# Kernel optimization log

Hardware: AMD Instinct MI355X
Metric: run time of the kernel (lower is better)

The kernel has to match this reference:

```python
import jax, jax.numpy as jnp
import numpy as np
import math

B, T, F = 1024, 120, 32          # batch, lookback, num_features
D, H, L = 128, 4, 2              # model_dim, heads, encoder layers
SD, RD, M, HOR = 16, 8, 5, 90    # symbol_dim, regime_dim, num_target_metrics, horizon
NSYM = 5000
HD = D // H

def _p(k, shape, scale=0.02):
    return (jax.random.normal(k, shape) * scale).astype(jnp.float32)

def _sinusoidal(seq_len, d_model):
    pos = jnp.arange(seq_len, dtype=jnp.float32)[:, None]
    div = jnp.exp(jnp.arange(0, d_model, 2, dtype=jnp.float32) * (-math.log(10000.0) / d_model))
    pe = jnp.zeros((seq_len, d_model), jnp.float32)
    pe = pe.at[:, 0::2].set(jnp.sin(pos * div))
    pe = pe.at[:, 1::2].set(jnp.cos(pos * div))
    return pe

def _ln(x, w, b, eps=1e-5):
    m = x.mean(-1, keepdims=True)
    v = jnp.var(x, axis=-1, keepdims=True)
    return (x - m) * jax.lax.rsqrt(v + eps) * w + b

def _mha(x, wqkv, bqkv, wo, bo):
    b, t, d = x.shape
    qkv = x @ wqkv.T + bqkv                      # [B,T,3D]
    q, k, v = jnp.split(qkv, 3, axis=-1)
    heads = lambda u: u.reshape(b, t, H, HD).transpose(0, 2, 1, 3)
    q, k, v = heads(q), heads(k), heads(v)       # [B,H,T,HD]
    s = jnp.einsum('bhqd,bhkd->bhqk', q, k) / jnp.sqrt(jnp.float32(HD))
    a = jax.nn.softmax(s, axis=-1)
    o = jnp.einsum('bhqk,bhkd->bhqd', a, v).transpose(0, 2, 1, 3).reshape(b, t, d)
    return o @ wo.T + bo

def setup_inputs():
    ks = iter(jax.random.split(jax.random.key(0), 40))
    return {
        'x': jax.random.normal(next(ks), (B, T, F), jnp.float32),
        'sym_id': jax.random.randint(next(ks), (B,), 0, NSYM),
        'regime_id': jax.random.randint(next(ks), (B,), 0, 3),
        'sym_emb': _p(next(ks), (NSYM, SD), 1.0),
        'reg_emb': _p(next(ks), (3, RD), 1.0),
        'in_w': _p(next(ks), (D, F + SD)), 'in_b': jnp.zeros((D,), jnp.float32),
        'enc_qkv_w': _p(next(ks), (L, 3 * D, D)), 'enc_qkv_b': jnp.zeros((L, 3 * D), jnp.float32),
        'enc_out_w': _p(next(ks), (L, D, D)), 'enc_out_b': jnp.zeros((L, D), jnp.float32),
        'enc_ln1_w': jnp.ones((L, D), jnp.float32), 'enc_ln1_b': jnp.zeros((L, D), jnp.float32),
        'enc_ln2_w': jnp.ones((L, D), jnp.float32), 'enc_ln2_b': jnp.zeros((L, D), jnp.float32),
        'enc_f1_w': _p(next(ks), (L, 4 * D, D)), 'enc_f1_b': jnp.zeros((L, 4 * D), jnp.float32),
        'enc_f2_w': _p(next(ks), (L, D, 4 * D)), 'enc_f2_b': jnp.zeros((L, D), jnp.float32),
        'pool_w': _p(next(ks), (1, D)), 'pool_b': jnp.zeros((1,), jnp.float32),
        'ctx_w': _p(next(ks), (D, D + SD + RD)), 'ctx_b': jnp.zeros((D,), jnp.float32),
        'gru_wih': _p(next(ks), (3 * D, M + D)), 'gru_whh': _p(next(ks), (3 * D, D)),
        'gru_bih': jnp.zeros((3 * D,), jnp.float32), 'gru_bhh': jnp.zeros((3 * D,), jnp.float32),
        'mu_w1': _p(next(ks), (64, D)), 'mu_b1': jnp.zeros((64,), jnp.float32),
        'mu_w2': _p(next(ks), (M, 64)), 'mu_b2': jnp.zeros((M,), jnp.float32),
        'vol_w1': _p(next(ks), (64, D)), 'vol_b1': jnp.zeros((64,), jnp.float32),
        'vol_w2': _p(next(ks), (M, 64)), 'vol_b2': jnp.zeros((M,), jnp.float32),
    }

def reference(x, sym_id, regime_id, sym_emb, reg_emb, in_w, in_b,
              enc_qkv_w, enc_qkv_b, enc_out_w, enc_out_b,
              enc_ln1_w, enc_ln1_b, enc_ln2_w, enc_ln2_b,
              enc_f1_w, enc_f1_b, enc_f2_w, enc_f2_b,
              pool_w, pool_b, ctx_w, ctx_b,
              gru_wih, gru_whh, gru_bih, gru_bhh,
              mu_w1, mu_b1, mu_w2, mu_b2, vol_w1, vol_b1, vol_w2, vol_b2):
    b = x.shape[0]
    se = sym_emb[sym_id]                                        # [B,SD]
    sym_seq = jnp.broadcast_to(se[:, None, :], (b, T, SD))
    feats = jnp.concatenate([x, sym_seq], axis=-1) @ in_w.T + in_b
    feats = feats + _sinusoidal(T, D)[None]
    # pre-LN transformer encoder (PyTorch norm_first=True, relu FFN, eval mode: no dropout)
    h = feats
    for l in range(L):
        y = _ln(h, enc_ln1_w[l], enc_ln1_b[l])
        h = h + _mha(y, enc_qkv_w[l], enc_qkv_b[l], enc_out_w[l], enc_out_b[l])
        y = _ln(h, enc_ln2_w[l], enc_ln2_b[l])
        h = h + (jax.nn.relu(y @ enc_f1_w[l].T + enc_f1_b[l]) @ enc_f2_w[l].T + enc_f2_b[l])
    attn_w = jax.nn.softmax(h @ pool_w.T + pool_b, axis=1)      # softmax over time
    pooled = (attn_w * h).sum(axis=1)                           # [B,D]
    re = reg_emb[regime_id]
    ctx = jnp.concatenate([pooled, se, re], axis=-1) @ ctx_w.T + ctx_b
    rv = jnp.std(x[:, :, 0], axis=1, ddof=1, keepdims=True)     # unbiased std like torch.std, [B,1]
    gelu = lambda t: jax.nn.gelu(t, approximate=False)          # torch nn.GELU default (erf)

    def step_fn(carry, _):
        hd, step = carry
        gi = jnp.concatenate([step, ctx], axis=-1) @ gru_wih.T + gru_bih
        gh = hd @ gru_whh.T + gru_bhh
        ir, iz, inn = jnp.split(gi, 3, axis=-1)
        hr, hz, hn = jnp.split(gh, 3, axis=-1)
        r = jax.nn.sigmoid(ir + hr)
        z = jax.nn.sigmoid(iz + hz)
        n = jnp.tanh(inn + r * hn)
        hd = (1.0 - z) * n + z * hd
        mu = jnp.tanh(gelu(hd @ mu_w1.T + mu_b1) @ mu_w2.T + mu_b2)
        sig = jax.nn.softplus(gelu(hd @ vol_w1.T + vol_b1) @ vol_w2.T + vol_b2) * (1.0 + rv)
        pred = mu * sig
        return (hd, pred), pred

    (_, _), preds = jax.lax.scan(step_fn, (ctx, jnp.zeros((b, M), x.dtype)), None, length=HOR)
    return preds.transpose(1, 0, 2)                             # [B,HOR,M]
```

## Files before the change

### kernel.cpp

```cpp
#include <hip/hip_runtime.h>
#include <math.h>

typedef __bf16 bf16;
typedef __bf16 bf16x8 __attribute__((ext_vector_type(8)));
typedef __bf16 bf16x2 __attribute__((ext_vector_type(2)));
typedef float  floatx4 __attribute__((ext_vector_type(4)));

#define BB 1024
#define TT 120
#define FF 32
#define DD 128
#define NROWS (BB*TT)
#define HOR 90
#define MM 5

__device__ __forceinline__ float fast_sigmoid(float x) {
    x = fminf(fmaxf(x, -30.f), 30.f);
    return 1.f / (1.f + __expf(-x));
}
__device__ __forceinline__ float fast_tanh(float x) {
    x = fminf(fmaxf(x, -15.f), 15.f);
    float e = __expf(-2.f * x);
    return (1.f - e) / (1.f + e);
}

__global__ __launch_bounds__(256) void prep_weights(
    const float* __restrict__ qkv, const float* __restrict__ outw,
    const float* __restrict__ f1,  const float* __restrict__ f2,
    bf16* __restrict__ dst)
{
    int i = blockIdx.x*256 + threadIdx.x;
    if (i >= 393216) return;
    float v;
    if      (i < 98304)  v = qkv[i];
    else if (i < 131072) v = outw[i - 98304];
    else if (i < 262144) v = f1[i - 131072];
    else                 v = f2[i - 262144];
    dst[i] = (bf16)v;
}

__global__ __launch_bounds__(256) void inproj3(
    const float* __restrict__ x, const int* __restrict__ sym_id,
    const float* __restrict__ sym_emb, const float* __restrict__ in_w,
    const float* __restrict__ in_b, const float* __restrict__ lnw,
    const float* __restrict__ lnb, float* __restrict__ h, bf16* __restrict__ y)
{
    __shared__ float xin[4][48];
    const int tid = threadIdx.x, lane = tid & 63, wave = tid >> 6;
    const int row0 = blockIdx.x * 4;
    if (tid < 192) {
        int rr = tid / 48, k = tid % 48;
        int row = row0 + rr;
        int b = row / TT;
        xin[rr][k] = (k < 32) ? x[(size_t)row*FF + k]
                              : sym_emb[(size_t)sym_id[b]*16 + (k - 32)];
    }
    __syncthreads();
    const int row = row0 + wave;
    const int t = row % TT;
    const int d0 = lane*2;
    float a0 = in_b[d0], a1 = in_b[d0+1];
    const float* w0 = in_w + (size_t)d0*48;
    const float* w1 = w0 + 48;
    #pragma unroll 8
    for (int k = 0; k < 48; ++k) {
        float xv = xin[wave][k];
        a0 += xv * w0[k];
        a1 += xv * w1[k];
    }
    const float f = expf((float)d0 * (-9.210340371976184f / 128.f));
    const float arg = (float)t * f;
    a0 += sinf(arg);
    a1 += cosf(arg);
    float2 hv = {a0, a1};
    *(float2*)&h[(size_t)row*DD + d0] = hv;
    float s = a0 + a1, ss = a0*a0 + a1*a1;
    #pragma unroll
    for (int o = 1; o < 64; o <<= 1) { s += __shfl_xor(s, o); ss += __shfl_xor(ss, o); }
    float mean = s * (1.f/128.f);
    float var  = ss * (1.f/128.f) - mean*mean;
    float rstd = rsqrtf(var + 1e-5f);
    bf16x2 o2 = {(bf16)((a0 - mean)*rstd*lnw[d0]   + lnb[d0]),
                 (bf16)((a1 - mean)*rstd*lnw[d0+1] + lnb[d0+1])};
    *(bf16x2*)&y[(size_t)row*DD + d0] = o2;
}

template<int EPI>
__global__ __launch_bounds__(256) void gemm64(
    const bf16* __restrict__ A, const bf16* __restrict__ W,
    const float* __restrict__ bias, const float* __restrict__ res,
    void* __restrict__ outp, const float* __restrict__ lnw,
    const float* __restrict__ lnb, bf16* __restrict__ yout, int N, int K)
{
    __shared__ alignas(16) bf16 As[128*64];
    __shared__ alignas(16) bf16 Ws[128*64];
    __shared__ float psum[2][128];
    __shared__ float psq[2][128];
    const int tid = threadIdx.x;
    const int lane = tid & 63, wave = tid >> 6;
    const int q = lane >> 4, ml = lane & 15;
    const int wm = (wave & 1) * 64, wn = (wave >> 1) * 64;
    const int m0 = blockIdx.x * 128, n0 = blockIdx.y * 128;
    floatx4 acc[4][4];
    #pragma unroll
    for (int i = 0; i < 4; ++i)
        #pragma unroll
        for (int j = 0; j < 4; ++j) acc[i][j] = (floatx4){0.f,0.f,0.f,0.f};
    const int nkb = K >> 6;
    for (int kb = 0; kb < nkb; ++kb) {
        #pragma unroll
        for (int i = 0; i < 4; ++i) {
            int idx = i*256 + tid;
            int r = idx >> 3, c = idx & 7;
            int sw = ((c ^ (r & 7)) * 8);
            *(uint4*)&As[r*64 + sw] = *(const uint4*)(A + (size_t)(m0 + r)*K + kb*64 + c*8);
            *(uint4*)&Ws[r*64 + sw] = *(const uint4*)(W + (size_t)(n0 + r)*K + kb*64 + c*8);
        }
        __syncthreads();
        #pragma unroll
        for (int s = 0; s < 2; ++s) {
            bf16x8 af[4], bfr[4];
            #pragma unroll
            for (int t = 0; t < 4; ++t) {
                int ra = wm + t*16 + ml;
                af[t]  = *(const bf16x8*)&As[ra*64 + (((s*4+q) ^ (ra & 7))*8)];
                int rb = wn + t*16 + ml;
                bfr[t] = *(const bf16x8*)&Ws[rb*64 + (((s*4+q) ^ (rb & 7))*8)];
            }
            #pragma unroll
            for (int i = 0; i < 4; ++i)
                #pragma unroll
                for (int j = 0; j < 4; ++j)
                    acc[i][j] = __builtin_amdgcn_mfma_f32_16x16x32_bf16(af[i], bfr[j], acc[i][j], 0, 0, 0);
        }
        __syncthreads();
    }
    #pragma unroll
    for (int j = 0; j < 4; ++j) {
        int col = n0 + wn + j*16 + ml;
        float bv = bias[col];
        #pragma unroll
        for (int i = 0; i < 4; ++i) {
            #pragma unroll
            for (int r = 0; r < 4; ++r) {
                int row = m0 + wm + i*16 + q*4 + r;
                size_t o = (size_t)row * N + col;
                float v = acc[i][j][r] + bv;
                if      (EPI == 0) ((bf16*)outp)[o] = (bf16)v;
                else if (EPI == 1) ((bf16*)outp)[o] = (bf16)fmaxf(v, 0.f);
                else {
                    v += res[o];
                    ((float*)outp)[o] = v;
                    acc[i][j][r] = v;
                }
            }
        }
    }
    if (EPI == 3) {
        float lw[4], lb[4];
        #pragma unroll
        for (int j = 0; j < 4; ++j) { int col = wn + j*16 + ml; lw[j] = lnw[col]; lb[j] = lnb[col]; }
        #pragma unroll
        for (int i = 0; i < 4; ++i)
            #pragma unroll
            for (int r = 0; r < 4; ++r) {
                float s  = acc[i][0][r] + acc[i][1][r] + acc[i][2][r] + acc[i][3][r];
                float ss = acc[i][0][r]*acc[i][0][r] + acc[i][1][r]*acc[i][1][r]
                         + acc[i][2][r]*acc[i][2][r] + acc[i][3][r]*acc[i][3][r];
                #pragma unroll
                for (int o = 1; o < 16; o <<= 1) { s += __shfl_xor(s, o); ss += __shfl_xor(ss, o); }
                if (ml == 0) {
                    int row = wm + i*16 + q*4 + r;
                    psum[wn >> 6][row] = s;
                    psq [wn >> 6][row] = ss;
                }
            }
        __syncthreads();
        #pragma unroll
        for (int i = 0; i < 4; ++i)
            #pragma unroll
            for (int r = 0; r < 4; ++r) {
                int row = wm + i*16 + q*4 + r;
                float mean = (psum[0][row] + psum[1][row]) * (1.f/128.f);
                float var  = (psq[0][row] + psq[1][row]) * (1.f/128.f) - mean*mean;
                float rstd = rsqrtf(var + 1e-5f);
                #pragma unroll
                for (int j = 0; j < 4; ++j) {
                    int col = wn + j*16 + ml;
                    yout[(size_t)(m0 + row)*128 + col] =
                        (bf16)((acc[i][j][r] - mean)*rstd*lw[j] + lb[j]);
                }
            }
    }
}

template<int LNFUSE>
__global__ __launch_bounds__(256) void ffn_fused(
    const bf16* __restrict__ y, const bf16* __restrict__ W1,
    const float* __restrict__ b1, const bf16* __restrict__ W2,
    const float* __restrict__ b2, float* __restrict__ h,
    const float* __restrict__ lnw, const float* __restrict__ lnb,
    bf16* __restrict__ yout)
{
    __shared__ alignas(16) bf16 ys[64*128];
    __shared__ alignas(16) bf16 mid[4][64*128];
    __shared__ alignas(16) bf16 wbuf[128*128];
    const int tid = threadIdx.x;
    const int lane = tid & 63, wave = tid >> 6;
    const int q = lane >> 4, ml = lane & 15;
    const int wm = wave * 16;
    const int m0 = blockIdx.x * 64;
    #pragma unroll
    for (int i = 0; i < 4; ++i) {
        int idx = i*256 + tid;
        int r = idx >> 4, cc = idx & 15;
        *(uint4*)&ys[r*128 + ((cc ^ (r & 15))*8)] =
            *(const uint4*)(y + (size_t)(m0 + r)*128 + cc*8);
    }
    __syncthreads();
    for (int nb = 0; nb < 4; ++nb) {
        #pragma unroll
        for (int i = 0; i < 8; ++i) {
            int idx = i*256 + tid;
            int r = idx >> 4, cc = idx & 15;
            *(uint4*)&wbuf[r*128 + ((cc ^ (r & 15))*8)] =
                *(const uint4*)(W1 + (size_t)(nb*128 + r)*128 + cc*8);
        }
        __syncthreads();
        bf16x8 af[4];
        #pragma unroll
        for (int s = 0; s < 4; ++s) {
            int ra = wm + ml;
            af[s] = *(const bf16x8*)&ys[ra*128 + (((4*s+q) ^ (ra & 15))*8)];
        }
        #pragma unroll
        for (int j = 0; j < 8; ++j) {
            floatx4 acc = (floatx4){0.f,0.f,0.f,0.f};
            #pragma unroll
            for (int s = 0; s < 4; ++s) {
                int rb = j*16 + ml;
                bf16x8 bfr = *(const bf16x8*)&wbuf[rb*128 + (((4*s+q) ^ (rb & 15))*8)];
                acc = __builtin_amdgcn_mfma_f32_16x16x32_bf16(af[s], bfr, acc, 0, 0, 0);
            }
            int col = j*16 + ml;
            float bv = b1[nb*128 + col];
            #pragma unroll
            for (int r = 0; r < 4; ++r) {
                int row = wm + q*4 + r;
                float v = fmaxf(acc[r] + bv, 0.f);
                mid[nb][row*128 + (((col>>3) ^ (row & 15))*8) + (col & 7)] = (bf16)v;
            }
        }
        __syncthreads();
    }
    floatx4 acc2[8];
    #pragma unroll
    for (int j = 0; j < 8; ++j) acc2[j] = (floatx4){0.f,0.f,0.f,0.f};
    for (int kb = 0; kb < 4; ++kb) {
        #pragma unroll
        for (int i = 0; i < 8; ++i) {
            int idx = i*256 + tid;
            int r = idx >> 4, cc = idx & 15;
            *(uint4*)&wbuf[r*128 + ((cc ^ (r & 15))*8)] =
                *(const uint4*)(W2 + (size_t)r*512 + kb*128 + cc*8);
        }
        __syncthreads();
        bf16x8 af[4];
        #pragma unroll
        for (int s = 0; s < 4; ++s) {
            int ra = wm + ml;
            af[s] = *(const bf16x8*)&mid[kb][ra*128 + (((4*s+q) ^ (ra & 15))*8)];
        }
        #pragma unroll
        for (int j = 0; j < 8; ++j) {
            #pragma unroll
            for (int s = 0; s < 4; ++s) {
                int rb = j*16 + ml;
                bf16x8 bfr = *(const bf16x8*)&wbuf[rb*128 + (((4*s+q) ^ (rb & 15))*8)];
                acc2[j] = __builtin_amdgcn_mfma_f32_16x16x32_bf16(af[s], bfr, acc2[j], 0, 0, 0);
            }
        }
        __syncthreads();
    }
    float vr[8][4];
    #pragma unroll
    for (int j = 0; j < 8; ++j) {
        int col = j*16 + ml;
        float bv = b2[col];
        #pragma unroll
        for (int r = 0; r < 4; ++r) {
            int row = wm + q*4 + r;
            size_t o = (size_t)(m0 + row)*128 + col;
            float v = acc2[j][r] + bv + h[o];
            h[o] = v;
            vr[j][r] = v;
        }
    }
    if (LNFUSE) {
        float lw[8], lb[8];
        #pragma unroll
        for (int j = 0; j < 8; ++j) { lw[j] = lnw[j*16 + ml]; lb[j] = lnb[j*16 + ml]; }
        #pragma unroll
        for (int r = 0; r < 4; ++r) {
            float s = 0.f, ss = 0.f;
            #pragma unroll
            for (int j = 0; j < 8; ++j) { s += vr[j][r]; ss += vr[j][r]*vr[j][r]; }
            #pragma unroll
            for (int o = 1; o < 16; o <<= 1) { s += __shfl_xor(s, o); ss += __shfl_xor(ss, o); }
            float mean = s * (1.f/128.f);
            float var  = ss * (1.f/128.f) - mean*mean;
            float rstd = rsqrtf(var + 1e-5f);
            int row = wm + q*4 + r;
            #pragma unroll
            for (int j = 0; j < 8; ++j)
                yout[(size_t)(m0 + row)*128 + j*16 + ml] =
                    (bf16)((vr[j][r] - mean)*rstd*lw[j] + lb[j]);
        }
    }
}

__global__ __launch_bounds__(256) void attn_b16(
    const bf16* __restrict__ qkv, bf16* __restrict__ O)
{
    __shared__ alignas(16) bf16 Qs[128*32];
    __shared__ alignas(16) bf16 Ks[128*32];
    __shared__ alignas(16) bf16 VT[32*128];
    __shared__ float Sf[64*132];
    const int tid = threadIdx.x, lane = tid & 63, wave = tid >> 6;
    const int q = lane >> 4, ml = lane & 15;
    const int b = blockIdx.x >> 2, hh = blockIdx.x & 3;
    const bf16* base = qkv + (size_t)b*TT*384 + hh*32;
    #pragma unroll
    for (int i = 0; i < 2; ++i) {
        int idx = i*256 + tid;
        int r = idx >> 2, cc = idx & 3;
        uint4 vq = {0,0,0,0}, vk = {0,0,0,0};
        if (r < TT) {
            vq = *(const uint4*)(base + (size_t)r*384 + cc*8);
            vk = *(const uint4*)(base + (size_t)r*384 + 128 + cc*8);
        }
        int cs = cc ^ ((r >> 1) & 3);
        *(uint4*)&Qs[r*32 + cs*8] = vq;
        *(uint4*)&Ks[r*32 + cs*8] = vk;
    }
    #pragma unroll
    for (int i = 0; i < 16; ++i) {
        int idx = i*256 + tid;
        int t = idx >> 5, e = idx & 31;
        bf16 v = (bf16)0.f;
        if (t < TT) v = base[(size_t)t*384 + 256 + e];
        VT[e*128 + (((t >> 3) ^ (e & 15))*8) + (t & 7)] = v;
    }
    __syncthreads();
    const float scale = 0.17677669529663687f;
    for (int hf = 0; hf < 2; ++hf) {
        {
            int rowa = hf*64 + wave*16 + ml;
            bf16x8 af = *(const bf16x8*)&Qs[rowa*32 + ((q ^ ((rowa>>1)&3))*8)];
            #pragma unroll
            for (int ni = 0; ni < 8; ++ni) {
                int rowb = ni*16 + ml;
                bf16x8 bfr = *(const bf16x8*)&Ks[rowb*32 + ((q ^ ((rowb>>1)&3))*8)];
                floatx4 a4 = __builtin_amdgcn_mfma_f32_16x16x32_bf16(
                    af, bfr, (floatx4){0.f,0.f,0.f,0.f}, 0, 0, 0);
                #pragma unroll
                for (int r = 0; r < 4; ++r)
                    Sf[(wave*16 + q*4 + r)*132 + ni*16 + ml] = a4[r]*scale;
            }
        }
        __syncthreads();
        {
            int rl = wave*16 + (lane >> 2);
            int part = lane & 3;
            int rg = hf*64 + rl;
            if (rg < TT) {
                float* rowp = &Sf[rl*132 + part*30];
                float mx = -3e38f;
                #pragma unroll 10
                for (int j = 0; j < 30; ++j) mx = fmaxf(mx, rowp[j]);
                mx = fmaxf(mx, __shfl_xor(mx, 1));
                mx = fmaxf(mx, __shfl_xor(mx, 2));
                float sm = 0.f;
                #pragma unroll 10
                for (int j = 0; j < 30; ++j) sm += __expf(rowp[j] - mx);
                sm += __shfl_xor(sm, 1);
                sm += __shfl_xor(sm, 2);
                float inv = 1.f / sm;
                #pragma unroll 10
                for (int j = 0; j < 30; ++j) rowp[j] = __expf(rowp[j] - mx) * inv;
                if (part == 3) {
                    #pragma unroll
                    for (int c = 120; c < 128; ++c) Sf[rl*132 + c] = 0.f;
                }
            }
        }
        __syncthreads();
        floatx4 pacc[2];
        pacc[0] = (floatx4){0.f,0.f,0.f,0.f};
        pacc[1] = (floatx4){0.f,0.f,0.f,0.f};
        #pragma unroll
        for (int s = 0; s < 4; ++s) {
            const float* pr = &Sf[(wave*16 + ml)*132 + 32*s + 8*q];
            float4 p0 = *(const float4*)pr;
            float4 p1 = *(const float4*)(pr + 4);
            bf16x8 af2 = {(bf16)p0.x,(bf16)p0.y,(bf16)p0.z,(bf16)p0.w,
                          (bf16)p1.x,(bf16)p1.y,(bf16)p1.z,(bf16)p1.w};
            #pragma unroll
            for (int nv = 0; nv < 2; ++nv) {
                int e = nv*16 + ml;
                bf16x8 bfr = *(const bf16x8*)&VT[e*128 + ((((4*s+q) ^ (e & 15)))*8)];
                pacc[nv] = __builtin_amdgcn_mfma_f32_16x16x32_bf16(af2, bfr, pacc[nv], 0, 0, 0);
            }
        }
        #pragma unroll
        for (int nv = 0; nv < 2; ++nv)
            #pragma unroll
            for (int r = 0; r < 4; ++r) {
                int row = hf*64 + wave*16 + q*4 + r;
                if (row < TT)
                    O[((size_t)b*TT + row)*DD + hh*32 + nv*16 + ml] = (bf16)pacc[nv][r];
            }
        __syncthreads();
    }
}

__global__ __launch_bounds__(128) void pool_ctx3(
    const float* __restrict__ h, const float* __restrict__ x,
    const int* __restrict__ sym_id, const int* __restrict__ regime_id,
    const float* __restrict__ sym_emb, const float* __restrict__ reg_emb,
    const float* __restrict__ pool_w, const float* __restrict__ pool_b,
    const float* __restrict__ ctx_w, const float* __restrict__ ctx_b,
    float* __restrict__ ctxf, float* __restrict__ rv)
{
    __shared__ float sc[120];
    __shared__ float aw[120];
    __shared__ float cat[152];
    const int b = blockIdx.x;
    const int tid = threadIdx.x, lane = tid & 63, wave = tid >> 6;
    const float* hb = h + (size_t)b*TT*DD;
    for (int t = wave*60; t < wave*60 + 60; ++t) {
        const float2* hp = (const float2*)(hb + t*DD);
        float2 v = hp[lane];
        float s = v.x * pool_w[lane*2] + v.y * pool_w[lane*2 + 1];
        #pragma unroll
        for (int o = 1; o < 64; o <<= 1) s += __shfl_xor(s, o);
        if (lane == 0) sc[t] = s + pool_b[0];
    }
    __syncthreads();
    if (wave == 0) {
        float v0 = sc[lane];
        float v1 = (lane < 56) ? sc[lane + 64] : -3e38f;
        float mx = fmaxf(v0, v1);
        #pragma unroll
        for (int o = 1; o < 64; o <<= 1) mx = fmaxf(mx, __shfl_xor(mx, o));
        float e0 = expf(v0 - mx);
        float e1 = (lane < 56) ? expf(v1 - mx) : 0.f;
        float sm = e0 + e1;
        #pragma unroll
        for (int o = 1; o < 64; o <<= 1) sm += __shfl_xor(sm, o);
        float inv = 1.f / sm;
        aw[lane] = e0 * inv;
        if (lane < 56) aw[lane + 64] = e1 * inv;
    } else {
        float v0 = x[((size_t)b*TT + lane)*FF];
        float v1 = (lane < 56) ? x[((size_t)b*TT + lane + 64)*FF] : 0.f;
        float s = v0 + v1;
        #pragma unroll
        for (int o = 1; o < 64; o <<= 1) s += __shfl_xor(s, o);
        float mean = s / 120.f;
        float d0 = v0 - mean, d1 = (lane < 56) ? (v1 - mean) : 0.f;
        float ss = d0*d0 + d1*d1;
        #pragma unroll
        for (int o = 1; o < 64; o <<= 1) ss += __shfl_xor(ss, o);
        if (lane == 0) rv[b] = sqrtf(ss / 119.f);
    }
    __syncthreads();
    {
        float p = 0.f;
        for (int t = 0; t < TT; ++t) p += aw[t] * hb[(size_t)t*DD + tid];
        cat[tid] = p;
    }
    if (tid < 16)      cat[128 + tid] = sym_emb[(size_t)sym_id[b]*16 + tid];
    else if (tid < 24) cat[144 + (tid-16)] = reg_emb[regime_id[b]*8 + (tid-16)];
    __syncthreads();
    float acc = ctx_b[tid];
    const float* wr = ctx_w + (size_t)tid*152;
    for (int j = 0; j < 152; ++j) acc += cat[j] * wr[j];
    ctxf[(size_t)b*128 + tid] = acc;
}

#define G1IDX(rr,c) ((rr)*132 + (c) + ((c)>>5))
__global__ __launch_bounds__(512, 1) void gru5_kernel(
    const float* __restrict__ ctxf, const float* __restrict__ wih,
    const float* __restrict__ bih, const float* __restrict__ whh,
    const float* __restrict__ bhh,
    const float* __restrict__ mu_w1, const float* __restrict__ mu_b1,
    const float* __restrict__ mu_w2, const float* __restrict__ mu_b2,
    const float* __restrict__ vol_w1, const float* __restrict__ vol_b1,
    const float* __restrict__ vol_w2, const float* __restrict__ vol_b2,
    const float* __restrict__ rv, float* __restrict__ out)
{
    __shared__ alignas(16) bf16 hdh[2][16*128];
    __shared__ alignas(16) bf16 hdl[2][16*128];
    __shared__ float g1_s[16*132];
    __shared__ float step_s[80];
    __shared__ float w2m_s[320], w2v_s[320];
    __shared__ float rvv[16];
    const int tid = threadIdx.x, lane = tid & 63, wave = tid >> 6;
    const int q = lane >> 4, ml = lane & 15;
    const int col = wave*16 + ml;
    const int r0 = blockIdx.x * 16;

    bf16x8 wbh1[3][4], wbl1[3][4], wbh2[4], wbl2[4];
    float w50[5], w51[5], w52[5];
    #pragma unroll
    for (int g = 0; g < 3; ++g) {
        int n = g*128 + col;
        #pragma unroll
        for (int s = 0; s < 4; ++s) {
            const float* wp = whh + (size_t)n*128 + s*32 + q*8;
            float4 f0 = *(const float4*)wp;
            float4 f1 = *(const float4*)(wp + 4);
            float v[8] = {f0.x,f0.y,f0.z,f0.w,f1.x,f1.y,f1.z,f1.w};
            bf16x8 hi, lo;
            #pragma unroll
            for (int j = 0; j < 8; ++j) {
                bf16 hb = (bf16)v[j]; hi[j] = hb; lo[j] = (bf16)(v[j] - (float)hb);
            }
            wbh1[g][s] = hi; wbl1[g][s] = lo;
        }
        #pragma unroll
        for (int j = 0; j < 5; ++j) {
            float wv = wih[(size_t)n*133 + j];
            if (g == 0) w50[j] = wv; else if (g == 1) w51[j] = wv; else w52[j] = wv;
        }
    }
    const float bhh0 = bhh[col], bhh1 = bhh[128 + col], bhh2 = bhh[256 + col];
    float bias2 = (col < 64) ? mu_b1[col] : vol_b1[col - 64];
    #pragma unroll
    for (int s = 0; s < 4; ++s) {
        const float* wp = ((col < 64) ? (mu_w1 + (size_t)col*128)
                                      : (vol_w1 + (size_t)(col-64)*128)) + s*32 + q*8;
        float4 f0 = *(const float4*)wp;
        float4 f1 = *(const float4*)(wp + 4);
        float v[8] = {f0.x,f0.y,f0.z,f0.w,f1.x,f1.y,f1.z,f1.w};
        bf16x8 hi, lo;
        #pragma unroll
        for (int j = 0; j < 8; ++j) {
            bf16 hb = (bf16)v[j]; hi[j] = hb; lo[j] = (bf16)(v[j] - (float)hb);
        }
        wbh2[s] = hi; wbl2[s] = lo;
    }

    for (int i = tid; i < 2048; i += 512) {
        int rr = i >> 7, d = i & 127;
        float v = ctxf[(size_t)r0*128 + i];
        g1_s[G1IDX(rr, d)] = v;
        int pos = rr*128 + (((d>>3) ^ rr) & 15)*8 + (d & 7);
        bf16 hb = (bf16)v;
        hdh[0][pos] = hb;
        hdl[0][pos] = (bf16)(v - (float)hb);
    }
    for (int i = tid; i < 320; i += 512) { w2m_s[i] = mu_w2[i]; w2v_s[i] = vol_w2[i]; }
    if (tid < 80) step_s[tid] = 0.f;
    if (tid < 16) rvv[tid] = 1.f + rv[r0 + tid];
    __syncthreads();
    float gi0[4], gi1[4], gi2[4];
    #pragma unroll
    for (int g = 0; g < 3; ++g) {
        int n = g*128 + col;
        const float* wr = wih + (size_t)n*133 + 5;
        #pragma unroll
        for (int r = 0; r < 4; ++r) {
            int row = q*4 + r;
            float a = bih[n];
            #pragma unroll 4
            for (int k = 0; k < 128; ++k) a += g1_s[G1IDX(row, k)] * wr[k];
            if (g == 0) gi0[r] = a; else if (g == 1) gi1[r] = a; else gi2[r] = a;
        }
    }
    __syncthreads();

    int cur = 0;
    for (int st = 0; st < HOR; ++st) {
        const int nxt = cur ^ 1;
        {
            bf16x8 ah[4], al[4];
            #pragma unroll
            for (int s = 0; s < 4; ++s) {
                int off = ml*128 + (((s*4 + q) ^ ml) & 15)*8;
                ah[s] = *(const bf16x8*)&hdh[cur][off];
                al[s] = *(const bf16x8*)&hdl[cur][off];
            }
            floatx4 a1 = (floatx4){0,0,0,0}, a2 = (floatx4){0,0,0,0}, a3 = (floatx4){0,0,0,0};
            floatx4 b1 = (floatx4){0,0,0,0}, b2 = (floatx4){0,0,0,0}, b3 = (floatx4){0,0,0,0};
            floatx4 c1 = (floatx4){0,0,0,0}, c2 = (floatx4){0,0,0,0}, c3 = (floatx4){0,0,0,0};
            #pragma unroll
            for (int s = 0; s < 4; ++s) {
                a1 = __builtin_amdgcn_mfma_f32_16x16x32_bf16(ah[s], wbh1[0][s], a1, 0, 0, 0);
                a2 = __builtin_amdgcn_mfma_f32_16x16x32_bf16(ah[s], wbl1[0][s], a2, 0, 0, 0);
                a3 = __builtin_amdgcn_mfma_f32_16x16x32_bf16(al[s], wbh1[0][s], a3, 0, 0, 0);
                b1 = __builtin_amdgcn_mfma_f32_16x16x32_bf16(ah[s], wbh1[1][s], b1, 0, 0, 0);
                b2 = __builtin_amdgcn_mfma_f32_16x16x32_bf16(ah[s], wbl1[1][s], b2, 0, 0, 0);
                b3 = __builtin_amdgcn_mfma_f32_16x16x32_bf16(al[s], wbh1[1][s], b3, 0, 0, 0);
                c1 = __builtin_amdgcn_mfma_f32_16x16x32_bf16(ah[s], wbh1[2][s], c1, 0, 0, 0);
                c2 = __builtin_amdgcn_mfma_f32_16x16x32_bf16(ah[s], wbl1[2][s], c2, 0, 0, 0);
                c3 = __builtin_amdgcn_mfma_f32_16x16x32_bf16(al[s], wbh1[2][s], c3, 0, 0, 0);
            }
            floatx4 ar = a1 + a2 + a3;
            floatx4 az = b1 + b2 + b3;
            floatx4 an = c1 + c2 + c3;
            #pragma unroll
            for (int r = 0; r < 4; ++r) {
                int row = q*4 + r;
                float ir = gi0[r], iz = gi1[r], in_ = gi2[r];
                #pragma unroll
                for (int j = 0; j < 5; ++j) {
                    float sv = step_s[row*5 + j];
                    ir  += sv * w50[j];
                    iz  += sv * w51[j];
                    in_ += sv * w52[j];
                }
                float rg = fast_sigmoid(ir + ar[r] + bhh0);
                float zg = fast_sigmoid(iz + az[r] + bhh1);
                float nn = fast_tanh(in_ + rg*(an[r] + bhh2));
                int pos = row*128 + (((col>>3) ^ row) & 15)*8 + (col & 7);
                float hold = (float)hdh[cur][pos] + (float)hdl[cur][pos];
                float hnew = (1.f - zg)*nn + zg*hold;
                bf16 hb = (bf16)hnew;
                hdh[nxt][pos] = hb;
                hdl[nxt][pos] = (bf16)(hnew - (float)hb);
            }
        }
        __syncthreads();
        {
            bf16x8 ah[4], al[4];
            #pragma unroll
            for (int s = 0; s < 4; ++s) {
                int off = ml*128 + (((s*4 + q) ^ ml) & 15)*8;
                ah[s] = *(const bf16x8*)&hdh[nxt][off];
                al[s] = *(const bf16x8*)&hdl[nxt][off];
            }
            floatx4 d1 = (floatx4){0,0,0,0}, d2 = (floatx4){0,0,0,0}, d3 = (floatx4){0,0,0,0};
            #pragma unroll
            for (int s = 0; s < 4; ++s) {
                d1 = __builtin_amdgcn_mfma_f32_16x16x32_bf16(ah[s], wbh2[s], d1, 0, 0, 0);
                d2 = __builtin_amdgcn_mfma_f32_16x16x32_bf16(ah[s], wbl2[s], d2, 0, 0, 0);
                d3 = __builtin_amdgcn_mfma_f32_16x16x32_bf16(al[s], wbh2[s], d3, 0, 0, 0);
            }
            floatx4 a4 = d1 + d2 + d3;
            #pragma unroll
            for (int r = 0; r < 4; ++r) {
                float u = a4[r] + bias2;
                g1_s[G1IDX(q*4 + r, col)] = 0.5f*u*(1.f + erff(u*0.70710678118654752f));
            }
        }
        __syncthreads();
        if (tid < 320) {
            int g = tid >> 2;
            int sub = tid & 3;
            int head = sub >> 1, half = sub & 1;
            int rr = g / 5, o = g % 5;
            const float* w2 = head ? w2v_s : w2m_s;
            int wb = o*64 + half*32;
            int gb = head*64 + half*32;
            float s = 0.f;
            #pragma unroll 8
            for (int j = 0; j < 32; ++j)
                s += g1_s[G1IDX(rr, gb + j)] * w2[wb + j];
            s += __shfl_xor(s, 1);
            float resv;
            if (head == 0) resv = tanhf(s + mu_b2[o]);
            else {
                float av = s + vol_b2[o];
                float sp = (av > 20.f) ? av : log1pf(expf(av));
                resv = sp * rvv[rr];
            }
            float other = __shfl_xor(resv, 2);
            if (sub == 0) {
                float pr = resv * other;
                step_s[g] = pr;
                out[((size_t)(r0 + rr)*HOR + st)*MM + o] = pr;
            }
        }
        __syncthreads();
        cur = nxt;
    }
}

extern "C" void kernel_launch(void* const* d_in, const int* in_sizes, int n_in,
                              void* d_out, int out_size, void* d_ws, size_t ws_size,
                              hipStream_t stream)
{
    (void)in_sizes; (void)n_in; (void)out_size;
    const float* x        = (const float*)d_in[0];
    const int*   sym_id   = (const int*)d_in[1];
    const int*   regime_id= (const int*)d_in[2];
    const float* sym_emb  = (const float*)d_in[3];
    const float* reg_emb  = (const float*)d_in[4];
    const float* in_w     = (const float*)d_in[5];
    const float* in_b     = (const float*)d_in[6];
    const float* qkv_w    = (const float*)d_in[7];
    const float* qkv_b    = (const float*)d_in[8];
    const float* out_w    = (const float*)d_in[9];
    const float* out_bv   = (const float*)d_in[10];
    const float* ln1_w    = (const float*)d_in[11];
    const float* ln1_b    = (const float*)d_in[12];
    const float* ln2_w    = (const float*)d_in[13];
    const float* ln2_b    = (const float*)d_in[14];
    const float* f1_w     = (const float*)d_in[15];
    const float* f1_b     = (const float*)d_in[16];
    const float* f2_w     = (const float*)d_in[17];
    const float* f2_b     = (const float*)d_in[18];
    const float* pool_w   = (const float*)d_in[19];
    const float* pool_b   = (const float*)d_in[20];
    const float* ctx_w    = (const float*)d_in[21];
    const float* ctx_b    = (const float*)d_in[22];
    const float* gru_wih  = (const float*)d_in[23];
    const float* gru_whh  = (const float*)d_in[24];
    const float* gru_bih  = (const float*)d_in[25];
    const float* gru_bhh  = (const float*)d_in[26];
    const float* mu_w1    = (const float*)d_in[27];
    const float* mu_b1    = (const float*)d_in[28];
    const float* mu_w2    = (const float*)d_in[29];
    const float* mu_b2    = (const float*)d_in[30];
    const float* vol_w1   = (const float*)d_in[31];
    const float* vol_b1   = (const float*)d_in[32];
    const float* vol_w2   = (const float*)d_in[33];
    const float* vol_b2   = (const float*)d_in[34];
    float* outp = (float*)d_out;

    char* ws = (char*)d_ws;
    size_t off = 0;
    auto alloc = [&](size_t bytes) -> void* {
        void* p = ws + off;
        off = (off + bytes + 255) & ~(size_t)255;
        return p;
    };
    float* h    = (float*)alloc((size_t)NROWS*DD*4);
    bf16*  y    = (bf16*) alloc((size_t)NROWS*DD*2);
    bf16*  wbf  = (bf16*) alloc((size_t)393216*2);
    float* ctxf = (float*)alloc((size_t)BB*DD*4);
    float* rv   = (float*)alloc((size_t)BB*4);
    size_t avail = (ws_size > off) ? (ws_size - off) : 0;
    int nch;
    if      (avail >= (size_t)NROWS*384*2)     nch = 1;
    else if (avail >= (size_t)NROWS/2*384*2)   nch = 2;
    else                                       nch = 4;
    const int RC = NROWS / nch;
    const int BC = BB / nch;
    bf16* big = (bf16*)(ws + off);

    prep_weights<<<1536, 256, 0, stream>>>(qkv_w, out_w, f1_w, f2_w, wbf);
    inproj3<<<NROWS/4, 256, 0, stream>>>(x, sym_id, sym_emb, in_w, in_b,
                                         ln1_w, ln1_b, h, y);

    for (int l = 0; l < 2; ++l) {
        const bf16* wqkv = wbf + l*49152;
        const bf16* wout = wbf + 98304 + l*16384;
        const bf16* wf1  = wbf + 131072 + l*65536;
        const bf16* wf2  = wbf + 262144 + l*65536;
        for (int c = 0; c < nch; ++c) {
            const size_t ro = (size_t)c*RC;
            gemm64<0><<<dim3(RC/128, 3), 256, 0, stream>>>(
                y + ro*DD, wqkv, qkv_b + l*384, nullptr, big,
                nullptr, nullptr, nullptr, 384, 128);
            attn_b16<<<BC*4, 256, 0, stream>>>(big, y + ro*DD);
        }
        gemm64<3><<<dim3(NROWS/128, 1), 256, 0, stream>>>(
            y, wout, out_bv + l*128, h, h, ln2_w + l*128, ln2_b + l*128, y, 128, 128);
        if (l == 0)
            ffn_fused<1><<<NROWS/64, 256, 0, stream>>>(
                y, wf1, f1_b, wf2, f2_b, h, ln1_w + 128, ln1_b + 128, y);
        else
            ffn_fused<0><<<NROWS/64, 256, 0, stream>>>(
                y, wf1, f1_b + 512, wf2, f2_b + 128, h, nullptr, nullptr, y);
    }

    pool_ctx3<<<BB, 128, 0, stream>>>(h, x, sym_id, regime_id, sym_emb, reg_emb,
                                      pool_w, pool_b, ctx_w, ctx_b, ctxf, rv);
    gru5_kernel<<<64, 512, 0, stream>>>(ctxf, gru_wih, gru_bih, gru_whh, gru_bhh,
                                        mu_w1, mu_b1, mu_w2, mu_b2,
                                        vol_w1, vol_b1, vol_w2, vol_b2,
                                        rv, outp);
}
```

Before: 1.491 ms.

## Halve FFN mid buffer, vectorize attention loads, use fast GRU head math

The fused FFN now interleaves its two GEMMs in halves, so only two 64x128 intermediate tiles sit in shared memory instead of four. This cuts LDS use and may allow more resident blocks, at the cost of extra barriers. The attention kernel drops the Q shared buffer, reading Q fragments straight from global memory, and loads V with 16-byte vector reads before scattering the transpose. The decoder replaces tanhf and log1pf(expf) with fast intrinsics, which lowers accuracy slightly.

```diff
diff --git a/kernel.cpp b/kernel.cpp
--- a/kernel.cpp
+++ b/kernel.cpp
@@ -203,7 +203,7 @@
     bf16* __restrict__ yout)
 {
     __shared__ alignas(16) bf16 ys[64*128];
-    __shared__ alignas(16) bf16 mid[4][64*128];
+    __shared__ alignas(16) bf16 mid[2][64*128];
     __shared__ alignas(16) bf16 wbuf[128*128];
     const int tid = threadIdx.x;
     const int lane = tid & 63, wave = tid >> 6;
@@ -217,70 +217,73 @@
         *(uint4*)&ys[r*128 + ((cc ^ (r & 15))*8)] =
             *(const uint4*)(y + (size_t)(m0 + r)*128 + cc*8);
     }
-    __syncthreads();
-    for (int nb = 0; nb < 4; ++nb) {
-        #pragma unroll
-        for (int i = 0; i < 8; ++i) {
-            int idx = i*256 + tid;
-            int r = idx >> 4, cc = idx & 15;
-            *(uint4*)&wbuf[r*128 + ((cc ^ (r & 15))*8)] =
-                *(const uint4*)(W1 + (size_t)(nb*128 + r)*128 + cc*8);
-        }
-        __syncthreads();
-        bf16x8 af[4];
-        #pragma unroll
-        for (int s = 0; s < 4; ++s) {
-            int ra = wm + ml;
-            af[s] = *(const bf16x8*)&ys[ra*128 + (((4*s+q) ^ (ra & 15))*8)];
-        }
-        #pragma unroll
-        for (int j = 0; j < 8; ++j) {
-            floatx4 acc = (floatx4){0.f,0.f,0.f,0.f};
+    floatx4 acc2[8];
+    #pragma unroll
+    for (int j = 0; j < 8; ++j) acc2[j] = (floatx4){0.f,0.f,0.f,0.f};
+    for (int half = 0; half < 2; ++half) {
+        for (int j2 = 0; j2 < 2; ++j2) {
+            int nb = half*2 + j2;
+            __syncthreads();
+            #pragma unroll
+            for (int i = 0; i < 8; ++i) {
+                int idx = i*256 + tid;
+                int r = idx >> 4, cc = idx & 15;
+                *(uint4*)&wbuf[r*128 + ((cc ^ (r & 15))*8)] =
+                    *(const uint4*)(W1 + (size_t)(nb*128 + r)*128 + cc*8);
+            }
+            __syncthreads();
+            bf16x8 af[4];
             #pragma unroll
             for (int s = 0; s < 4; ++s) {
-                int rb = j*16 + ml;
-                bf16x8 bfr = *(const bf16x8*)&wbuf[rb*128 + (((4*s+q) ^ (rb & 15))*8)];
-                acc = __builtin_amdgcn_mfma_f32_16x16x32_bf16(af[s], bfr, acc, 0, 0, 0);
-            }
-            int col = j*16 + ml;
-            float bv = b1[nb*128 + col];
-            #pragma unroll
-            for (int r = 0; r < 4; ++r) {
-                int row = wm + q*4 + r;
-                float v = fmaxf(acc[r] + bv, 0.f);
-                mid[nb][row*128 + (((col>>3) ^ (row & 15))*8) + (col & 7)] = (bf16)v;
-            }
-        }
-        __syncthreads();
-    }
-    floatx4 acc2[8];
-    #pragma unroll
-    for (int j = 0; j < 8; ++j) acc2[j] = (floatx4){0.f,0.f,0.f,0.f};
-    for (int kb = 0; kb < 4; ++kb) {
-        #pragma unroll
-        for (int i = 0; i < 8; ++i) {
-            int idx = i*256 + tid;
-            int r = idx >> 4, cc = idx & 15;
-            *(uint4*)&wbuf[r*128 + ((cc ^ (r & 15))*8)] =
-                *(const uint4*)(W2 + (size_t)r*512 + kb*128 + cc*8);
-        }
-        __syncthreads();
-        bf16x8 af[4];
-        #pragma unroll
-        for (int s = 0; s < 4; ++s) {
-            int ra = wm + ml;
-            af[s] = *(const bf16x8*)&mid[kb][ra*128 + (((4*s+q) ^ (ra & 15))*8)];
-        }
-        #pragma unroll
-        for (int j = 0; j < 8; ++j) {
+                int ra = wm + ml;
+                af[s] = *(const bf16x8*)&ys[ra*128 + (((4*s+q) ^ (ra & 15))*8)];
+            }
+            #pragma unroll
+            for (int j = 0; j < 8; ++j) {
+                floatx4 acc = (floatx4){0.f,0.f,0.f,0.f};
+                #pragma unroll
+                for (int s = 0; s < 4; ++s) {
+                    int rb = j*16 + ml;
+                    bf16x8 bfr = *(const bf16x8*)&wbuf[rb*128 + (((4*s+q) ^ (rb & 15))*8)];
+                    acc = __builtin_amdgcn_mfma_f32_16x16x32_bf16(af[s], bfr, acc, 0, 0, 0);
+                }
+                int col = j*16 + ml;
+                float bv = b1[nb*128 + col];
+                #pragma unroll
+                for (int r = 0; r < 4; ++r) {
+                    int row = wm + q*4 + r;
+                    float v = fmaxf(acc[r] + bv, 0.f);
+                    mid[j2][row*128 + (((col>>3) ^ (row & 15))*8) + (col & 7)] = (bf16)v;
+                }
+            }
+        }
+        for (int j2 = 0; j2 < 2; ++j2) {
+            int kb = half*2 + j2;
+            __syncthreads();
+            #pragma unroll
+            for (int i = 0; i < 8; ++i) {
+                int idx = i*256 + tid;
+                int r = idx >> 4, cc = idx & 15;
+                *(uint4*)&wbuf[r*128 + ((cc ^ (r & 15))*8)] =
+                    *(const uint4*)(W2 + (size_t)r*512 + kb*128 + cc*8);
+            }
+            __syncthreads();
+            bf16x8 af[4];
             #pragma unroll
             for (int s = 0; s < 4; ++s) {
-                int rb = j*16 + ml;
-                bf16x8 bfr = *(const bf16x8*)&wbuf[rb*128 + (((4*s+q) ^ (rb & 15))*8)];
-                acc2[j] = __builtin_amdgcn_mfma_f32_16x16x32_bf16(af[s], bfr, acc2[j], 0, 0, 0);
-            }
-        }
-        __syncthreads();
+                int ra = wm + ml;
+                af[s] = *(const bf16x8*)&mid[j2][ra*128 + (((4*s+q) ^ (ra & 15))*8)];
+            }
+            #pragma unroll
+            for (int j = 0; j < 8; ++j) {
+                #pragma unroll
+                for (int s = 0; s < 4; ++s) {
+                    int rb = j*16 + ml;
+                    bf16x8 bfr = *(const bf16x8*)&wbuf[rb*128 + (((4*s+q) ^ (rb & 15))*8)];
+                    acc2[j] = __builtin_amdgcn_mfma_f32_16x16x32_bf16(af[s], bfr, acc2[j], 0, 0, 0);
+                }
+            }
+        }
     }
     float vr[8][4];
     #pragma unroll
@@ -322,7 +325,6 @@
 __global__ __launch_bounds__(256) void attn_b16(
     const bf16* __restrict__ qkv, bf16* __restrict__ O)
 {
-    __shared__ alignas(16) bf16 Qs[128*32];
     __shared__ alignas(16) bf16 Ks[128*32];
     __shared__ alignas(16) bf16 VT[32*128];
     __shared__ float Sf[64*132];
@@ -334,29 +336,39 @@
     for (int i = 0; i < 2; ++i) {
         int idx = i*256 + tid;
         int r = idx >> 2, cc = idx & 3;
-        uint4 vq = {0,0,0,0}, vk = {0,0,0,0};
-        if (r < TT) {
-            vq = *(const uint4*)(base + (size_t)r*384 + cc*8);
-            vk = *(const uint4*)(base + (size_t)r*384 + 128 + cc*8);
-        }
+        uint4 vk = {0,0,0,0};
+        if (r < TT) vk = *(const uint4*)(base + (size_t)r*384 + 128 + cc*8);
         int cs = cc ^ ((r >> 1) & 3);
-        *(uint4*)&Qs[r*32 + cs*8] = vq;
         *(uint4*)&Ks[r*32 + cs*8] = vk;
     }
-    #pragma unroll
-    for (int i = 0; i < 16; ++i) {
+    {
+        int e = tid >> 3, t = 120 + (tid & 7);
+        VT[e*128 + (((t >> 3) ^ (e & 15))*8) + (t & 7)] = (bf16)0.f;
+    }
+    #pragma unroll
+    for (int i = 0; i < 2; ++i) {
         int idx = i*256 + tid;
-        int t = idx >> 5, e = idx & 31;
-        bf16 v = (bf16)0.f;
-        if (t < TT) v = base[(size_t)t*384 + 256 + e];
-        VT[e*128 + (((t >> 3) ^ (e & 15))*8) + (t & 7)] = v;
+        if (idx < 480) {
+            int t = idx >> 2, c = idx & 3;
+            uint4 vv = *(const uint4*)(base + (size_t)t*384 + 256 + c*8);
+            bf16 tmp[8];
+            *(uint4*)tmp = vv;
+            #pragma unroll
+            for (int jj = 0; jj < 8; ++jj) {
+                int e = c*8 + jj;
+                VT[e*128 + (((t >> 3) ^ (e & 15))*8) + (t & 7)] = tmp[jj];
+            }
+        }
     }
     __syncthreads();
     const float scale = 0.17677669529663687f;
     for (int hf = 0; hf < 2; ++hf) {
         {
             int rowa = hf*64 + wave*16 + ml;
-            bf16x8 af = *(const bf16x8*)&Qs[rowa*32 + ((q ^ ((rowa>>1)&3))*8)];
+            bf16x8 af;
+            #pragma unroll
+            for (int j = 0; j < 8; ++j) af[j] = (bf16)0.f;
+            if (rowa < TT) af = *(const bf16x8*)(base + (size_t)rowa*384 + q*8);
             #pragma unroll
             for (int ni = 0; ni < 8; ++ni) {
                 int rowb = ni*16 + ml;
@@ -670,10 +682,10 @@
                 s += g1_s[G1IDX(rr, gb + j)] * w2[wb + j];
             s += __shfl_xor(s, 1);
             float resv;
-            if (head == 0) resv = tanhf(s + mu_b2[o]);
+            if (head == 0) resv = fast_tanh(s + mu_b2[o]);
             else {
                 float av = s + vol_b2[o];
-                float sp = (av > 20.f) ? av : log1pf(expf(av));
+                float sp = (av > 20.f) ? av : __logf(1.f + __expf(av));
                 resv = sp * rvv[rr];
             }
             float other = __shfl_xor(resv, 2);
```

Result: faster. 1.357 ms (-9.0%).
